# Optimization experiments

Hardware: AMD Instinct MI355X
Metric: run time of the kernel (lower is better)

## Reference

```python
import jax, jax.numpy as jnp
import numpy as np

D_MODEL = 1024
N_HEADS = 16
D_K = D_MODEL // N_HEADS
D_FF = 4096
EPS = 1e-5


def _linear_params(key, d_in, d_out):
    kw, kb = jax.random.split(key)
    lim = 1.0 / np.sqrt(d_in)
    W = jax.random.uniform(kw, (d_in, d_out), jnp.float32, -lim, lim)
    b = jax.random.uniform(kb, (d_out,), jnp.float32, -lim, lim)
    return W, b


def setup_inputs() -> dict:
    key = jax.random.key(0)
    ks = jax.random.split(key, 8)
    x = jax.random.normal(ks[0], (4, 2048, D_MODEL), jnp.float32)
    wq, bq = _linear_params(ks[1], D_MODEL, D_MODEL)
    wk, bk = _linear_params(ks[2], D_MODEL, D_MODEL)
    wv, bv = _linear_params(ks[3], D_MODEL, D_MODEL)
    wo, bo = _linear_params(ks[4], D_MODEL, D_MODEL)
    w1, b1 = _linear_params(ks[5], D_MODEL, D_FF)
    w2, b2 = _linear_params(ks[6], D_FF, D_MODEL)
    g1 = jnp.ones((D_MODEL,), jnp.float32)
    be1 = jnp.zeros((D_MODEL,), jnp.float32)
    g2 = jnp.ones((D_MODEL,), jnp.float32)
    be2 = jnp.zeros((D_MODEL,), jnp.float32)
    return dict(x=x, wq=wq, bq=bq, wk=wk, bk=bk, wv=wv, bv=bv, wo=wo, bo=bo,
                w1=w1, b1=b1, w2=w2, b2=b2, g1=g1, be1=be1, g2=g2, be2=be2)


def _layernorm(x, gamma, beta):
    mu = jnp.mean(x, axis=-1, keepdims=True)
    var = jnp.mean(jnp.square(x - mu), axis=-1, keepdims=True)
    return (x - mu) * jax.lax.rsqrt(var + EPS) * gamma + beta


def _encoder_layer(x, wq, bq, wk, bk, wv, bv, wo, bo, w1, b1, w2, b2, g1, be1, g2, be2):
    B, S, _ = x.shape
    # QKV projections, split into heads: (B, H, S, d_k)
    def split_heads(t):
        return t.reshape(B, S, N_HEADS, D_K).transpose(0, 2, 1, 3)
    q = split_heads(x @ wq + bq)
    k = split_heads(x @ wk + bk)
    v = split_heads(x @ wv + bv)
    scores = jnp.einsum('bhqd,bhkd->bhqk', q, k) / np.sqrt(D_K).astype(np.float32)
    attn = jax.nn.softmax(scores, axis=-1)
    ctx = jnp.einsum('bhqk,bhkd->bhqd', attn, v)
    ctx = ctx.transpose(0, 2, 1, 3).reshape(B, S, D_MODEL)
    attn_out = ctx @ wo + bo
    x = _layernorm(x + attn_out, g1, be1)
    ff = jax.nn.relu(x @ w1 + b1) @ w2 + b2
    x = _layernorm(x + ff, g2, be2)
    return x


def reference(x, wq, bq, wk, bk, wv, bv, wo, bo, w1, b1, w2, b2, g1, be1, g2, be2):
    return _encoder_layer(x, wq, bq, wk, bk, wv, bv, wo, bo, w1, b1, w2, b2, g1, be1, g2, be2)
```

## Files before the change

### kernel.cpp

```cpp
#include <hip/hip_runtime.h>
#include <hip/hip_bf16.h>

#define DEV __device__ __forceinline__

typedef __attribute__((ext_vector_type(8))) short bf16x8;
typedef __attribute__((ext_vector_type(4))) float f32x4;

constexpr int B = 4, S = 2048, D = 1024, H = 16, DK = 64, DFF = 4096;
constexpr int NT = B * S;
constexpr int HS = B * H * S;
constexpr float QSCALE = 0.125f * 1.44269504088896f;

#if __has_builtin(__builtin_amdgcn_exp2f)
#define EXP2(x) __builtin_amdgcn_exp2f(x)
#else
#define EXP2(x) exp2f(x)
#endif

DEV unsigned short f2bf(float f) {
  return __builtin_bit_cast(unsigned short, __float2bfloat16(f));
}
DEV float bf2f(unsigned short u) { return __uint_as_float((unsigned)u << 16); }

DEV void gld16(unsigned short* ldsbase, const unsigned short* g, int lane) {
#if __has_builtin(__builtin_amdgcn_global_load_lds)
  __builtin_amdgcn_global_load_lds((const __attribute__((address_space(1))) unsigned int*)g,
                                   (__attribute__((address_space(3))) unsigned int*)ldsbase,
                                   16, 0, 0);
#else
  *(uint4*)(ldsbase + lane * 8) = *(const uint4*)g;
#endif
}

__global__ __launch_bounds__(256) void cvt_bf16_kernel(const float* __restrict__ in,
                                                       unsigned short* __restrict__ out, int n) {
  int i = (blockIdx.x * 256 + threadIdx.x) * 8;
  if (i >= n) return;
  float4 a = *(const float4*)(in + i);
  float4 b = *(const float4*)(in + i + 4);
  uint4 o;
  o.x = f2bf(a.x) | ((unsigned)f2bf(a.y) << 16);
  o.y = f2bf(a.z) | ((unsigned)f2bf(a.w) << 16);
  o.z = f2bf(b.x) | ((unsigned)f2bf(b.y) << 16);
  o.w = f2bf(b.z) | ((unsigned)f2bf(b.w) << 16);
  *(uint4*)(out + i) = o;
}

__global__ __launch_bounds__(256) void transpose_cvt_all_kernel(
    const float* __restrict__ wq, const float* __restrict__ wk, const float* __restrict__ wv,
    const float* __restrict__ wo, const float* __restrict__ w1, const float* __restrict__ w2,
    unsigned short* __restrict__ wqkvT, unsigned short* __restrict__ woT,
    unsigned short* __restrict__ w1T, unsigned short* __restrict__ w2T) {
  __shared__ unsigned short tile[64][72];
  int bid = blockIdx.x;
  const float* in;
  unsigned short* out;
  int R, C, tb;
  if (bid < 1024) {
    int wsel = bid >> 8;
    tb = bid & 255;
    R = 1024; C = 1024;
    in = wsel == 0 ? wq : wsel == 1 ? wk : wsel == 2 ? wv : wo;
    out = wsel < 3 ? wqkvT + (size_t)wsel * D * D : woT;
  } else if (bid < 2048) {
    tb = bid - 1024; R = 1024; C = 4096; in = w1; out = w1T;
  } else {
    tb = bid - 2048; R = 4096; C = 1024; in = w2; out = w2T;
  }
  int gx = C >> 6;
  int rb = (tb / gx) * 64, cb = (tb % gx) * 64;
  int t = threadIdx.x;
#pragma unroll
  for (int i = 0; i < 16; ++i) {
    int c = t + i * 256;
    int r = c >> 6, cc = c & 63;
    tile[cc][r] = f2bf(in[(size_t)(rb + r) * C + cb + cc]);
  }
  __syncthreads();
#pragma unroll
  for (int i = 0; i < 16; ++i) {
    int c = t + i * 256;
    int rr = c >> 6, cc = c & 63;
    out[(size_t)(cb + rr) * R + rb + cc] = tile[rr][cc];
  }
}

template <int BNW, int OMODE, bool RELU>
__global__ __launch_bounds__(512) void gemm256_kernel(const unsigned short* __restrict__ A,
                                                      const unsigned short* __restrict__ WT,
                                                      const float* __restrict__ bias0,
                                                      const float* __restrict__ bias1,
                                                      const float* __restrict__ bias2,
                                                      const unsigned short* __restrict__ res,
                                                      void* __restrict__ out0,
                                                      void* __restrict__ out1,
                                                      void* __restrict__ out2,
                                                      int M, int N, int K) {
  constexpr int BN = BNW * 64;
  __shared__ __align__(16) unsigned short sA[2][256 * 64];
  __shared__ __align__(16) unsigned short sB[2][BN * 64];

  int t = threadIdx.x, w = t >> 6, l = t & 63;
  int ll = l & 15, lh = l >> 4;

  int lin = blockIdx.x, nwg = gridDim.x;
  int wg = (nwg & 7) == 0 ? (lin & 7) * (nwg >> 3) + (lin >> 3) : lin;
  int gx = N / BN;
  int bn = wg % gx, bm = wg / gx;

  const int wm = (w >> 2) * 128, wn = (w & 3) * (BNW * 16);

  f32x4 acc[8][BNW] = {};

  const int srow = w * 8 + (l >> 3);
  const int sunit = (l & 7) ^ ((l >> 3) & 7);
  const unsigned short* gA = A + ((size_t)bm * 256 + srow) * K + sunit * 8;
  const unsigned short* gB = WT + ((size_t)bn * BN + srow) * K + sunit * 8;

  auto stage = [&](int buf, int kb) {
#pragma unroll
    for (int i = 0; i < 4; ++i)
      gld16(&sA[buf][(i * 64 + w * 8) * 64], gA + (size_t)(i * 64) * K + kb, l);
#pragma unroll
    for (int i = 0; i < BN / 64; ++i)
      gld16(&sB[buf][(i * 64 + w * 8) * 64], gB + (size_t)(i * 64) * K + kb, l);
  };

  const int NK = K >> 6;
  stage(0, 0);
  stage(1, 64);

  for (int kt = 0; kt < NK; ++kt) {
    int cur = kt & 1;
    if (kt == NK - 1)
      asm volatile("s_waitcnt vmcnt(0)" ::: "memory");
    else if constexpr (BNW == 4)
      asm volatile("s_waitcnt vmcnt(8)" ::: "memory");
    else
      asm volatile("s_waitcnt vmcnt(6)" ::: "memory");
    __builtin_amdgcn_s_barrier();
    asm volatile("" ::: "memory");

    const unsigned short* cA = sA[cur];
    const unsigned short* cB = sB[cur];
#pragma unroll
    for (int kk = 0; kk < 2; ++kk) {
      bf16x8 af[8], bf[BNW];
#pragma unroll
      for (int mt = 0; mt < 8; ++mt) {
        int rr = wm + mt * 16 + ll;
        af[mt] = *(const bf16x8*)(&cA[rr * 64 + (((kk * 4 + lh) ^ (ll & 7)) * 8)]);
      }
#pragma unroll
      for (int nt = 0; nt < BNW; ++nt) {
        int rr = wn + nt * 16 + ll;
        bf[nt] = *(const bf16x8*)(&cB[rr * 64 + (((kk * 4 + lh) ^ (ll & 7)) * 8)]);
      }
      __builtin_amdgcn_s_setprio(1);
#pragma unroll
      for (int mt = 0; mt < 8; ++mt)
#pragma unroll
        for (int nt = 0; nt < BNW; ++nt)
          acc[mt][nt] = __builtin_amdgcn_mfma_f32_16x16x32_bf16(af[mt], bf[nt], acc[mt][nt], 0, 0, 0);
      __builtin_amdgcn_s_setprio(0);
    }
    asm volatile("" ::: "memory");
    __builtin_amdgcn_s_barrier();
    asm volatile("" ::: "memory");
    if (kt + 2 < NK) stage(cur, (kt + 2) * 64);
  }

#pragma unroll
  for (int mt = 0; mt < 8; ++mt) {
#pragma unroll
    for (int nt = 0; nt < BNW; ++nt) {
      int col = bn * BN + wn + nt * 16 + ll;
      int row0 = bm * 256 + wm + mt * 16 + lh * 4;
      if constexpr (OMODE == 3) {
        int sec = col >> 10, c = col & 1023;
        float bv = (sec == 0 ? bias0 : (sec == 1 ? bias1 : bias2))[c];
        if (sec == 2) {
          int b_ = row0 >> 11, s_ = row0 & 2047;
          size_t vr = ((size_t)(b_ * H + (c >> 6)) * 64 + (c & 63)) * S + s_;
          uint2 pk;
          pk.x = (unsigned)f2bf(acc[mt][nt][0] + bv) | ((unsigned)f2bf(acc[mt][nt][1] + bv) << 16);
          pk.y = (unsigned)f2bf(acc[mt][nt][2] + bv) | ((unsigned)f2bf(acc[mt][nt][3] + bv) << 16);
          *(uint2*)((unsigned short*)out2 + vr) = pk;
        } else {
          unsigned short* o = sec == 0 ? (unsigned short*)out0 : (unsigned short*)out1;
          float sc_ = sec == 0 ? QSCALE : 1.f;
#pragma unroll
          for (int r = 0; r < 4; ++r)
            o[(size_t)(row0 + r) * 1024 + c] = f2bf((acc[mt][nt][r] + bv) * sc_);
        }
      } else {
        float bv = bias0[col];
#pragma unroll
        for (int r = 0; r < 4; ++r) {
          float v = acc[mt][nt][r] + bv;
          if (RELU) v = fmaxf(v, 0.f);
          if (OMODE == 4) {
            v += bf2f(res[(size_t)(row0 + r) * N + col]);
            ((unsigned short*)out0)[(size_t)(row0 + r) * N + col] = f2bf(v);
          } else if (OMODE == 1)
            ((unsigned short*)out0)[(size_t)(row0 + r) * N + col] = f2bf(v);
          else
            ((float*)out0)[(size_t)(row0 + r) * N + col] = v;
        }
      }
    }
  }
}

__global__ __launch_bounds__(512) void attn_kernel(const unsigned short* __restrict__ q,
                                                   const unsigned short* __restrict__ k,
                                                   const unsigned short* __restrict__ vt,
                                                   unsigned short* __restrict__ O1,
                                                   unsigned short* __restrict__ O2,
                                                   float* __restrict__ ml) {
  __shared__ __align__(16) unsigned short sK[2][64 * 64];
  __shared__ __align__(16) unsigned short sV[2][64 * 64];
  __shared__ __align__(16) unsigned short sP[8][16 * 72];
  int t = threadIdx.x, w = t >> 6, l = t & 63;
  int ll = l & 15, lh = l >> 4;
  int bh = blockIdx.y, hf = blockIdx.z;
  int q0 = blockIdx.x * 256 + w * 32;
  const size_t base = (size_t)(bh >> 4) * S * D + (size_t)(bh & 15) * DK;
  const size_t vtbase = (size_t)bh * 64 * S;
  unsigned short* Opart = hf ? O2 : O1;
  float* mlh = ml + (size_t)hf * 2 * HS;
  unsigned short* sPw = sP[w];

  const int srow = t >> 3;
  const int scol = 8 * ((t & 7) ^ (srow & 7));
  const unsigned short* gk = k + base + (size_t)srow * D + scol;
  const unsigned short* gv = vt + vtbase + (size_t)srow * S + scol;
  const int kb0 = hf * 1024;

  bf16x8 qf[2][2];
#pragma unroll
  for (int qs = 0; qs < 2; ++qs)
#pragma unroll
    for (int kk = 0; kk < 2; ++kk)
      qf[qs][kk] = *(const bf16x8*)(q + base + (size_t)(q0 + qs * 16 + ll) * D + kk * 32 + lh * 8);

  f32x4 cacc[2][4] = {};
  float m[2] = {-1e30f, -1e30f}, lsum[2] = {0.f, 0.f};

  const int swz = (ll & 7) << 3;

  gld16(&sK[0][w * 512], gk + (size_t)kb0 * D, l);
  gld16(&sV[0][w * 512], gv + kb0, l);
  asm volatile("s_waitcnt vmcnt(0)" ::: "memory");
  __syncthreads();

  int cur = 0;
  for (int step = 0; step < 16; ++step) {
    int kb = kb0 + step * 64;
    if (step < 15) {
      gld16(&sK[cur ^ 1][w * 512], gk + (size_t)(kb + 64) * D, l);
      gld16(&sV[cur ^ 1][w * 512], gv + (kb + 64), l);
    }
    const unsigned short* sKc = sK[cur];
    const unsigned short* sVc = sV[cur];

    bf16x8 kf[4][2];
#pragma unroll
    for (int nt = 0; nt < 4; ++nt)
#pragma unroll
      for (int kk = 0; kk < 2; ++kk)
        kf[nt][kk] = *(const bf16x8*)(sKc + (nt * 16 + ll) * 64 + ((kk * 32 + lh * 8) ^ swz));

    bf16x8 pf[2][2];
#pragma unroll
    for (int qs = 0; qs < 2; ++qs) {
      f32x4 sc[4] = {};
      __builtin_amdgcn_s_setprio(1);
#pragma unroll
      for (int nt = 0; nt < 4; ++nt) {
        sc[nt] = __builtin_amdgcn_mfma_f32_16x16x32_bf16(kf[nt][0], qf[qs][0], sc[nt], 0, 0, 0);
        sc[nt] = __builtin_amdgcn_mfma_f32_16x16x32_bf16(kf[nt][1], qf[qs][1], sc[nt], 0, 0, 0);
      }
      __builtin_amdgcn_s_setprio(0);
      float tm = -1e30f;
#pragma unroll
      for (int nt = 0; nt < 4; ++nt)
#pragma unroll
        for (int r = 0; r < 4; ++r) tm = fmaxf(tm, sc[nt][r]);
      tm = fmaxf(tm, __shfl_xor(tm, 16));
      tm = fmaxf(tm, __shfl_xor(tm, 32));
      if (!__all(tm <= m[qs] + 8.0f)) {
        float mn = fmaxf(m[qs], tm);
        float rsc = EXP2(m[qs] - mn);
        lsum[qs] *= rsc;
#pragma unroll
        for (int dt = 0; dt < 4; ++dt)
#pragma unroll
          for (int r = 0; r < 4; ++r) cacc[qs][dt][r] *= rsc;
        m[qs] = mn;
      }
      float p[4][4], ps = 0.f;
#pragma unroll
      for (int nt = 0; nt < 4; ++nt)
#pragma unroll
        for (int r = 0; r < 4; ++r) {
          p[nt][r] = EXP2(sc[nt][r] - m[qs]);
          ps += p[nt][r];
        }
      ps += __shfl_xor(ps, 16);
      ps += __shfl_xor(ps, 32);
      lsum[qs] += ps;
#pragma unroll
      for (int nt = 0; nt < 4; ++nt) {
        uint2 pk;
        pk.x = (unsigned)f2bf(p[nt][0]) | ((unsigned)f2bf(p[nt][1]) << 16);
        pk.y = (unsigned)f2bf(p[nt][2]) | ((unsigned)f2bf(p[nt][3]) << 16);
        *(uint2*)(&sPw[ll * 72 + nt * 16 + lh * 4]) = pk;
      }
      pf[qs][0] = *(const bf16x8*)(&sPw[ll * 72 + lh * 8]);
      pf[qs][1] = *(const bf16x8*)(&sPw[ll * 72 + 32 + lh * 8]);
    }

    bf16x8 vf[4][2];
#pragma unroll
    for (int dt = 0; dt < 4; ++dt)
#pragma unroll
      for (int kt = 0; kt < 2; ++kt)
        vf[dt][kt] = *(const bf16x8*)(sVc + (dt * 16 + ll) * 64 + ((kt * 32 + lh * 8) ^ swz));
    __builtin_amdgcn_s_setprio(1);
#pragma unroll
    for (int qs = 0; qs < 2; ++qs)
#pragma unroll
      for (int dt = 0; dt < 4; ++dt)
#pragma unroll
        for (int kt = 0; kt < 2; ++kt)
          cacc[qs][dt] = __builtin_amdgcn_mfma_f32_16x16x32_bf16(pf[qs][kt], vf[dt][kt], cacc[qs][dt], 0, 0, 0);
    __builtin_amdgcn_s_setprio(0);

    asm volatile("s_waitcnt vmcnt(0)" ::: "memory");
    __syncthreads();
    cur ^= 1;
  }

  int h64 = (bh & 15) * 64;
  int brow = (bh >> 4) * S;
#pragma unroll
  for (int qs = 0; qs < 2; ++qs) {
#pragma unroll
    for (int dt = 0; dt < 4; ++dt)
#pragma unroll
      for (int r = 0; r < 4; ++r) {
        int tok = brow + q0 + qs * 16 + lh * 4 + r;
        Opart[(size_t)tok * D + h64 + dt * 16 + ll] = f2bf(cacc[qs][dt][r]);
      }
    if (lh == 0) {
      int qq = q0 + qs * 16 + ll;
      mlh[(size_t)bh * S + qq] = m[qs];
      mlh[HS + (size_t)bh * S + qq] = lsum[qs];
    }
  }
}

__global__ __launch_bounds__(256) void attn_combine_kernel(const unsigned short* __restrict__ O1,
                                                           const unsigned short* __restrict__ O2,
                                                           const float* __restrict__ ml,
                                                           unsigned short* __restrict__ ctx) {
  int tok = blockIdx.x, tid = threadIdx.x;
  int h = tid >> 4;
  int bhs = ((tok >> 11) * H + h) * S + (tok & 2047);
  float m1 = ml[bhs], l1 = ml[HS + bhs];
  float m2 = ml[2 * HS + bhs], l2 = ml[3 * HS + bhs];
  float mm = fmaxf(m1, m2);
  float a1 = EXP2(m1 - mm), a2 = EXP2(m2 - mm);
  float inv = 1.f / (a1 * l1 + a2 * l2);
  a1 *= inv; a2 *= inv;
  size_t idx = (size_t)tok * D + tid * 4;
  ushort4 u1 = *(const ushort4*)(O1 + idx);
  ushort4 u2 = *(const ushort4*)(O2 + idx);
  uint2 pk;
  pk.x = (unsigned)f2bf(a1 * bf2f(u1.x) + a2 * bf2f(u2.x)) |
         ((unsigned)f2bf(a1 * bf2f(u1.y) + a2 * bf2f(u2.y)) << 16);
  pk.y = (unsigned)f2bf(a1 * bf2f(u1.z) + a2 * bf2f(u2.z)) |
         ((unsigned)f2bf(a1 * bf2f(u1.w) + a2 * bf2f(u2.w)) << 16);
  *(uint2*)(ctx + idx) = pk;
}

template <bool OUT_F32>
__global__ __launch_bounds__(256) void ln_kernel(const unsigned short* __restrict__ a,
                                                 const float* __restrict__ gamma,
                                                 const float* __restrict__ beta,
                                                 float* __restrict__ outf,
                                                 unsigned short* __restrict__ outb) {
  __shared__ float sred[8];
  size_t row = blockIdx.x;
  int t = threadIdx.x;
  size_t bidx = row * D + t * 4;
  ushort4 u = *(const ushort4*)(a + bidx);
  float4 x;
  x.x = bf2f(u.x); x.y = bf2f(u.y); x.z = bf2f(u.z); x.w = bf2f(u.w);

  float s = x.x + x.y + x.z + x.w;
#pragma unroll
  for (int msk = 32; msk; msk >>= 1) s += __shfl_xor(s, msk);
  if ((t & 63) == 0) sred[t >> 6] = s;
  __syncthreads();
  float mu = (sred[0] + sred[1] + sred[2] + sred[3]) * (1.f / D);

  float dx = x.x - mu, dy = x.y - mu, dz = x.z - mu, dw = x.w - mu;
  float sq = dx * dx + dy * dy + dz * dz + dw * dw;
#pragma unroll
  for (int msk = 32; msk; msk >>= 1) sq += __shfl_xor(sq, msk);
  __syncthreads();
  if ((t & 63) == 0) sred[t >> 6] = sq;
  __syncthreads();
  float var = (sred[0] + sred[1] + sred[2] + sred[3]) * (1.f / D);
  float rs = rsqrtf(var + 1e-5f);

  float4 g = *(const float4*)(gamma + t * 4);
  float4 be = *(const float4*)(beta + t * 4);
  float4 y;
  y.x = dx * rs * g.x + be.x;
  y.y = dy * rs * g.y + be.y;
  y.z = dz * rs * g.z + be.z;
  y.w = dw * rs * g.w + be.w;
  if (OUT_F32) {
    *(float4*)(outf + bidx) = y;
  } else {
    uint2 o;
    o.x = (unsigned)f2bf(y.x) | ((unsigned)f2bf(y.y) << 16);
    o.y = (unsigned)f2bf(y.z) | ((unsigned)f2bf(y.w) << 16);
    *(uint2*)(outb + bidx) = o;
  }
}

extern "C" void kernel_launch(void* const* d_in, const int* in_sizes, int n_in,
                              void* d_out, int out_size, void* d_ws, size_t ws_size,
                              hipStream_t stream) {
  const float* x   = (const float*)d_in[0];
  const float* wq  = (const float*)d_in[1];
  const float* bq  = (const float*)d_in[2];
  const float* wk  = (const float*)d_in[3];
  const float* bk  = (const float*)d_in[4];
  const float* wv  = (const float*)d_in[5];
  const float* bv  = (const float*)d_in[6];
  const float* wo  = (const float*)d_in[7];
  const float* bo  = (const float*)d_in[8];
  const float* w1  = (const float*)d_in[9];
  const float* b1  = (const float*)d_in[10];
  const float* w2  = (const float*)d_in[11];
  const float* b2  = (const float*)d_in[12];
  const float* g1  = (const float*)d_in[13];
  const float* be1 = (const float*)d_in[14];
  const float* g2  = (const float*)d_in[15];
  const float* be2 = (const float*)d_in[16];

  char* ws = (char*)d_ws;
  size_t off = 0;
  auto alloc = [&](size_t bytes) {
    char* p = ws + off;
    off += (bytes + 255) & ~(size_t)255;
    return p;
  };

  unsigned short* wqkvT = (unsigned short*)alloc((size_t)3 * D * D * 2);
  unsigned short* woT = (unsigned short*)alloc((size_t)D * D * 2);
  unsigned short* w1T = (unsigned short*)alloc((size_t)D * DFF * 2);
  unsigned short* w2T = (unsigned short*)alloc((size_t)DFF * D * 2);
  unsigned short* xb  = (unsigned short*)alloc((size_t)NT * D * 2);
  unsigned short* big = (unsigned short*)alloc((size_t)NT * DFF * 2);
  unsigned short* qb  = big;
  unsigned short* kb_ = big + (size_t)NT * D;
  unsigned short* ctb = big + (size_t)2 * NT * D;
  unsigned short* vtb = big + (size_t)3 * NT * D;
  unsigned short* O1  = (unsigned short*)alloc((size_t)NT * D * 2);
  unsigned short* O2  = (unsigned short*)alloc((size_t)NT * D * 2);
  float* mlbuf    = (float*)alloc((size_t)4 * HS * 4);
  unsigned short* x1b = xb;
  unsigned short* ffb = big;
  unsigned short* attn_out = O1;
  unsigned short* ff2 = O2;
  (void)ws_size; (void)in_sizes; (void)n_in; (void)out_size;

  cvt_bf16_kernel<<<NT * D / 2048, 256, 0, stream>>>(x, xb, NT * D);
  transpose_cvt_all_kernel<<<3072, 256, 0, stream>>>(wq, wk, wv, wo, w1, w2,
                                                     wqkvT, woT, w1T, w2T);

  gemm256_kernel<4, 3, false><<<(3 * D / 256) * (NT / 256), 512, 0, stream>>>(
      xb, wqkvT, bq, bk, bv, nullptr, qb, kb_, vtb, NT, 3 * D, D);

  attn_kernel<<<dim3(S / 256, B * H, 2), 512, 0, stream>>>(qb, kb_, vtb, O1, O2, mlbuf);
  attn_combine_kernel<<<NT, 256, 0, stream>>>(O1, O2, mlbuf, ctb);

  gemm256_kernel<2, 4, false><<<(D / 128) * (NT / 256), 512, 0, stream>>>(
      ctb, woT, bo, nullptr, nullptr, xb, attn_out, nullptr, nullptr, NT, D, D);

  ln_kernel<false><<<NT, 256, 0, stream>>>(attn_out, g1, be1, nullptr, x1b);

  gemm256_kernel<4, 1, true><<<(DFF / 256) * (NT / 256), 512, 0, stream>>>(
      x1b, w1T, b1, nullptr, nullptr, nullptr, ffb, nullptr, nullptr, NT, DFF, D);
  gemm256_kernel<2, 4, false><<<(D / 128) * (NT / 256), 512, 0, stream>>>(
      ffb, w2T, b2, nullptr, nullptr, x1b, ff2, nullptr, nullptr, NT, D, DFF);

  ln_kernel<true><<<NT, 256, 0, stream>>>(ff2, g2, be2, (float*)d_out, nullptr);
}
```

Before: 422.0 us.

## Restructure GEMM mainloop into 8-phase half-K pipelined schedule with finer LDS staging

Splits each 64-wide K tile of the LDS buffers into two 32-wide halves and rewrites the GEMM main loop as eight phases per two K tiles. Each phase loads a quarter of the A fragments and issues one chunk of global-to-LDS prefetch before its MFMAs, so memory traffic is interleaved with compute rather than issued in one burst. The LDS swizzle changes to match the 32-element rows. The cost is two barriers per phase and more complex vmcnt bookkeeping, and the extra synchronisation could stall the waves.

After: 419.2 us. No clear change (-0.7%).

```diff
diff --git a/kernel.cpp b/kernel.cpp
--- a/kernel.cpp
+++ b/kernel.cpp
@@ -16,6 +16,11 @@
 #else
 #define EXP2(x) exp2f(x)
 #endif
+
+#define BARRIER()                         \
+  asm volatile("" ::: "memory");          \
+  __builtin_amdgcn_s_barrier();           \
+  asm volatile("" ::: "memory")
 
 DEV unsigned short f2bf(float f) {
   return __builtin_bit_cast(unsigned short, __float2bfloat16(f));
@@ -97,8 +102,8 @@
                                                       void* __restrict__ out2,
                                                       int M, int N, int K) {
   constexpr int BN = BNW * 64;
-  __shared__ __align__(16) unsigned short sA[2][256 * 64];
-  __shared__ __align__(16) unsigned short sB[2][BN * 64];
+  __shared__ __align__(16) unsigned short sA[2][2][256 * 32];
+  __shared__ __align__(16) unsigned short sB[2][2][BN * 32];
 
   int t = threadIdx.x, w = t >> 6, l = t & 63;
   int ll = l & 15, lh = l >> 4;
@@ -109,65 +114,80 @@
   int bn = wg % gx, bm = wg / gx;
 
   const int wm = (w >> 2) * 128, wn = (w & 3) * (BNW * 16);
+  const int ua = (lh ^ ((ll >> 1) & 3)) * 8;
 
   f32x4 acc[8][BNW] = {};
 
-  const int srow = w * 8 + (l >> 3);
-  const int sunit = (l & 7) ^ ((l >> 3) & 7);
-  const unsigned short* gA = A + ((size_t)bm * 256 + srow) * K + sunit * 8;
-  const unsigned short* gB = WT + ((size_t)bn * BN + srow) * K + sunit * 8;
-
-  auto stage = [&](int buf, int kb) {
-#pragma unroll
-    for (int i = 0; i < 4; ++i)
-      gld16(&sA[buf][(i * 64 + w * 8) * 64], gA + (size_t)(i * 64) * K + kb, l);
-#pragma unroll
-    for (int i = 0; i < BN / 64; ++i)
-      gld16(&sB[buf][(i * 64 + w * 8) * 64], gB + (size_t)(i * 64) * K + kb, l);
+  const int pr = t >> 2, up = t & 3;
+  const int ulog = up ^ ((pr >> 1) & 3);
+  const unsigned short* gA0 = A + ((size_t)bm * 256 + pr) * K + ulog * 8;
+  const unsigned short* gB0 = WT + ((size_t)bn * BN + pr) * K + ulog * 8;
+
+  auto stgA = [&](int buf, int kh, int tile) {
+    const unsigned short* s = gA0 + (size_t)tile * 64 + kh * 32;
+    gld16(&sA[buf][kh][w * 512], s, l);
+    gld16(&sA[buf][kh][4096 + w * 512], s + (size_t)128 * K, l);
   };
+  auto stgB = [&](int buf, int kh, int tile) {
+    const unsigned short* s = gB0 + (size_t)tile * 64 + kh * 32;
+    gld16(&sB[buf][kh][w * 512], s, l);
+    if constexpr (BNW == 4) gld16(&sB[buf][kh][4096 + w * 512], s + (size_t)128 * K, l);
+  };
 
   const int NK = K >> 6;
-  stage(0, 0);
-  stage(1, 64);
-
-  for (int kt = 0; kt < NK; ++kt) {
-    int cur = kt & 1;
-    if (kt == NK - 1)
-      asm volatile("s_waitcnt vmcnt(0)" ::: "memory");
-    else if constexpr (BNW == 4)
-      asm volatile("s_waitcnt vmcnt(8)" ::: "memory");
-    else
-      asm volatile("s_waitcnt vmcnt(6)" ::: "memory");
-    __builtin_amdgcn_s_barrier();
-    asm volatile("" ::: "memory");
-
-    const unsigned short* cA = sA[cur];
-    const unsigned short* cB = sB[cur];
-#pragma unroll
-    for (int kk = 0; kk < 2; ++kk) {
-      bf16x8 af[8], bf[BNW];
-#pragma unroll
-      for (int mt = 0; mt < 8; ++mt) {
-        int rr = wm + mt * 16 + ll;
-        af[mt] = *(const bf16x8*)(&cA[rr * 64 + (((kk * 4 + lh) ^ (ll & 7)) * 8)]);
-      }
-#pragma unroll
-      for (int nt = 0; nt < BNW; ++nt) {
-        int rr = wn + nt * 16 + ll;
-        bf[nt] = *(const bf16x8*)(&cB[rr * 64 + (((kk * 4 + lh) ^ (ll & 7)) * 8)]);
-      }
+  stgA(0, 0, 0); stgB(0, 0, 0);
+  stgA(0, 1, 0); stgB(0, 1, 0);
+  stgA(1, 0, 1); stgB(1, 0, 1);
+  if constexpr (BNW == 4) asm volatile("s_waitcnt vmcnt(4)" ::: "memory");
+  else                    asm volatile("s_waitcnt vmcnt(3)" ::: "memory");
+  BARRIER();
+
+  bf16x8 bfr[BNW];
+  for (int it = 0; it < NK; it += 2) {
+    const bool more = it + 2 < NK;
+#pragma unroll
+    for (int ph = 0; ph < 8; ++ph) {
+      const int tb = ph >> 2;
+      const int kh = (ph >> 1) & 1;
+      const int mq = ph & 1;
+      bf16x8 af[4];
+      if (mq == 0) {
+#pragma unroll
+        for (int nt = 0; nt < BNW; ++nt)
+          bfr[nt] = *(const bf16x8*)(&sB[tb][kh][(wn + nt * 16 + ll) * 32 + ua]);
+      }
+#pragma unroll
+      for (int i = 0; i < 4; ++i)
+        af[i] = *(const bf16x8*)(&sA[tb][kh][(wm + (mq * 4 + i) * 16 + ll) * 32 + ua]);
+      if (ph == 0) stgA(1, 1, it + 1);
+      else if (ph == 1) stgB(1, 1, it + 1);
+      else if (more) {
+        if (ph == 2) stgA(0, 0, it + 2);
+        else if (ph == 3) stgB(0, 0, it + 2);
+        else if (ph == 4) stgA(0, 1, it + 2);
+        else if (ph == 5) stgB(0, 1, it + 2);
+        else if (ph == 6) stgA(1, 0, it + 3);
+        else stgB(1, 0, it + 3);
+      }
+      BARRIER();
       __builtin_amdgcn_s_setprio(1);
 #pragma unroll
-      for (int mt = 0; mt < 8; ++mt)
+      for (int i = 0; i < 4; ++i)
 #pragma unroll
         for (int nt = 0; nt < BNW; ++nt)
-          acc[mt][nt] = __builtin_amdgcn_mfma_f32_16x16x32_bf16(af[mt], bf[nt], acc[mt][nt], 0, 0, 0);
+          acc[mq * 4 + i][nt] =
+              __builtin_amdgcn_mfma_f32_16x16x32_bf16(af[i], bfr[nt], acc[mq * 4 + i][nt], 0, 0, 0);
       __builtin_amdgcn_s_setprio(0);
+      if (ph == 3 || ph == 7) {
+        if (more) {
+          if constexpr (BNW == 4) asm volatile("s_waitcnt vmcnt(4)" ::: "memory");
+          else                    asm volatile("s_waitcnt vmcnt(3)" ::: "memory");
+        } else {
+          asm volatile("s_waitcnt vmcnt(0)" ::: "memory");
+        }
+      }
+      BARRIER();
     }
-    asm volatile("" ::: "memory");
-    __builtin_amdgcn_s_barrier();
-    asm volatile("" ::: "memory");
-    if (kt + 2 < NK) stage(cur, (kt + 2) * 64);
   }
 
 #pragma unroll
```
